# Kernel optimization log

Measured on AMD Instinct MI355X. Metric: run time of the kernel, lower is better.

The kernel has to match this reference:

```python
import jax, jax.numpy as jnp
import numpy as np
import math

_PI = math.pi

@jax.custom_vjp
def atan_spike(h):
    # Heaviside forward, ATan surrogate (alpha=2.0) backward
    return (h >= 0).astype(h.dtype)

def _atan_fwd(h):
    return (h >= 0).astype(h.dtype), h

def _atan_bwd(h, g):
    # d/dh [ (1/pi) atan(pi*h) + 1/2 ] = 1 / (1 + (pi*h)^2)
    return (g / (1.0 + (_PI * h) ** 2),)

atan_spike.defvjp(_atan_fwd, _atan_bwd)

def plif_scan(x, alpha, v_th):
    # x: [T, ...]; PLIF: v += alpha*(x - v); spike; hard reset to 0
    a = alpha.reshape(())
    def step(v, xt):
        v = v + a * (xt - v)
        s = atan_spike(v - v_th)
        v = v * (1.0 - s)
        return v, s
    v0 = jnp.zeros_like(x[0])
    _, spikes = jax.lax.scan(step, v0, x)
    return spikes

def setup_inputs() -> dict:
    key = jax.random.key(0)
    k1, k2, k3 = jax.random.split(key, 3)
    T, B, N, D, H = 4, 8, 1024, 512, 2048
    x = jax.random.normal(k1, (T, B, N, D), dtype=jnp.float32)
    W1 = jax.random.normal(k2, (H, D), dtype=jnp.float32) * (1.0 / math.sqrt(D))
    W2 = jax.random.normal(k3, (D, H), dtype=jnp.float32) * (1.0 / math.sqrt(H))
    alpha1 = jnp.full((1,), 0.5, dtype=jnp.float32)  # 1/tau, tau=2.0
    alpha2 = jnp.full((1,), 0.5, dtype=jnp.float32)
    return {"x": x, "W1": W1, "W2": W2, "alpha1": alpha1, "alpha2": alpha2}

def reference(x, W1, W2, alpha1, alpha2):
    V_TH = 1.0
    h = jnp.einsum('tbnd,hd->tbnh', x, W1)      # fc1 (no bias)
    s1 = plif_scan(h, alpha1, V_TH)             # PLIF neuron 1
    y = jnp.einsum('tbnh,dh->tbnd', s1, W2)     # fc2 (no bias)
    s2 = plif_scan(y, alpha2, V_TH)             # PLIF neuron 2
    return s2
```

## Files before the change

kernel.cpp:

```cpp
#include <hip/hip_runtime.h>

#define T_  4
#define BN_ 8192
#define D_  512
#define H_  2048

typedef float f4 __attribute__((ext_vector_type(4)));
typedef float f32x4 __attribute__((ext_vector_type(4)));
typedef _Float16 f16x8 __attribute__((ext_vector_type(8)));

__device__ __forceinline__ void split8(const f4 u0, const f4 u1, f16x8& hi, f16x8& lo) {
#pragma unroll
    for (int i = 0; i < 4; ++i) {
        _Float16 a = (_Float16)u0[i]; hi[i]     = a; lo[i]     = (_Float16)(u0[i] - (float)a);
        _Float16 b = (_Float16)u1[i]; hi[4 + i] = b; lo[4 + i] = (_Float16)(u1[i] - (float)b);
    }
}

__device__ __forceinline__ void spikes4_to_f16(unsigned b, unsigned& lo, unsigned& hi) {
    const unsigned p0 = (b & 0xFFu) | ((b & 0xFF00u) << 8);
    const unsigned p1 = ((b >> 16) & 0xFFu) | ((b >> 8) & 0xFF0000u);
    lo = p0 * 0x3C00u;
    hi = p1 * 0x3C00u;
}

__device__ __forceinline__ void glds16(const void* g, void* l) {
    __builtin_amdgcn_global_load_lds((const __attribute__((address_space(1))) unsigned int*)g,
                                     (__attribute__((address_space(3))) unsigned int*)l, 16, 0, 0);
}

__global__ __launch_bounds__(256)
void k_split(const float* __restrict__ x, _Float16* __restrict__ xs)
{
    const int b   = blockIdx.x;
    const int t   = b & 3;
    const int k0B = (b >> 2) & 15;
    const int bnB = b >> 6;
    const int kg  = threadIdx.x & 3;
    const int row = threadIdx.x >> 2;

    const float* src = x + ((size_t)t * BN_ + bnB * 64 + row) * D_ + k0B * 32 + kg * 8;
    const f4 u0 = *(const f4*)src;
    const f4 u1 = *(const f4*)(src + 4);
    f16x8 hi, lo;
    split8(u0, u1, hi, lo);

    const size_t base = ((size_t)(bnB * 16 + k0B) * 4 + t) * 4096;
    *(f16x8*)&xs[base +        kg * 512 + row * 8] = hi;
    *(f16x8*)&xs[base + 2048 + kg * 512 + row * 8] = lo;
}

__global__ __launch_bounds__(256)
void k_splitW(const float* __restrict__ W1, _Float16* __restrict__ w1s)
{
    const int gid = blockIdx.x * 256 + threadIdx.x;
    const int col = gid & 127;
    const int kg  = (gid >> 7) & 3;
    const int kb  = (gid >> 9) & 15;
    const int h0b = gid >> 13;

    const float* src = W1 + (size_t)(h0b * 128 + col) * D_ + kb * 32 + kg * 8;
    const f4 u0 = *(const f4*)src;
    const f4 u1 = *(const f4*)(src + 4);
    f16x8 hi, lo;
    split8(u0, u1, hi, lo);

    const size_t base = (size_t)(h0b * 16 + kb) * 8192;
    *(f16x8*)&w1s[base +        kg * 1024 + col * 8] = hi;
    *(f16x8*)&w1s[base + 4096 + kg * 1024 + col * 8] = lo;
}

__global__ __launch_bounds__(256)
void k_splitW2(const float* __restrict__ W2, _Float16* __restrict__ w2s)
{
    const int gid = blockIdx.x * 256 + threadIdx.x;
    const int col = gid & 127;
    const int kg  = (gid >> 7) & 3;
    const int kb  = (gid >> 9) & 63;
    const int d0b = gid >> 15;

    const float* src = W2 + (size_t)(d0b * 128 + col) * H_ + kb * 32 + kg * 8;
    const f4 u0 = *(const f4*)src;
    const f4 u1 = *(const f4*)(src + 4);
    f16x8 hi, lo;
    split8(u0, u1, hi, lo);

    const size_t base = (size_t)(d0b * 64 + kb) * 8192;
    *(f16x8*)&w2s[base +        kg * 1024 + col * 8] = hi;
    *(f16x8*)&w2s[base + 4096 + kg * 1024 + col * 8] = lo;
}

__global__ __launch_bounds__(256, 2)
void k_fc1b(const _Float16* __restrict__ xs, const _Float16* __restrict__ w1s,
            const float* __restrict__ alphap, unsigned char* __restrict__ s1)
{
    __shared__ _Float16 Ab[2][T_][2][4][64][8];

    const int tid  = threadIdx.x;
    const int lane = tid & 63;
    const int w    = tid >> 6;
    const int wr   = (w >> 1) * 32;
    const int wc   = (w & 1) * 64;

    const int gid   = blockIdx.x;
    const int panel = gid >> 8;
    const int h0i   = (gid >> 4) & 15;
    const int bnL   = gid & 15;
    const int bnB   = panel * 16 + bnL;
    const int bn0   = bnB * 64;
    const int h0    = h0i * 128;

    const int l15 = lane & 15;
    const int kgl = lane >> 4;
    const int lq  = kgl * 4;

    const float a1v = alphap[0];

    f32x4 acc[T_][2][4];
#pragma unroll
    for (int t = 0; t < T_; ++t)
#pragma unroll
        for (int m = 0; m < 2; ++m)
#pragma unroll
            for (int n = 0; n < 4; ++n) acc[t][m][n] = (f32x4){0.f, 0.f, 0.f, 0.f};

    const char* xbase = (const char*)xs + (size_t)bnB * 16 * 32768;
    const _Float16* bl = w1s + (size_t)h0i * (16 * 8192)
                             + (size_t)kgl * 1024 + (size_t)(wc + l15) * 8;

#define FC1_GLDS(BUF, KB)                                                        \
    {                                                                            \
        const char* cb_ = xbase + (size_t)(KB) * 32768;                          \
        _Float16* lA_ = &Ab[BUF][0][0][0][0][0];                                 \
        _Pragma("unroll")                                                        \
        for (int i_ = 0; i_ < 8; ++i_) {                                         \
            const int c_ = i_ * 4 + w;                                           \
            glds16(cb_ + c_ * 1024 + lane * 16, lA_ + c_ * 512);                 \
        }                                                                        \
    }

#define FC1_BLOAD(KB, B0, B1)                                                    \
    {                                                                            \
        const _Float16* bp_ = bl + (size_t)(KB) * 8192;                          \
        _Pragma("unroll")                                                        \
        for (int n_ = 0; n_ < 4; ++n_) {                                         \
            B0[n_] = *(const f16x8*)(bp_ + n_ * 128);                            \
            B1[n_] = *(const f16x8*)(bp_ + 4096 + n_ * 128);                     \
        }                                                                        \
    }

#define FC1_COMPUTE(BUF, B0, B1)                                                 \
    _Pragma("unroll")                                                            \
    for (int t_ = 0; t_ < T_; ++t_)                                              \
        _Pragma("unroll")                                                        \
        for (int m_ = 0; m_ < 2; ++m_) {                                         \
            const f16x8 a0_ = *(const f16x8*)&Ab[BUF][t_][0][kgl][wr + m_ * 16 + l15][0]; \
            const f16x8 a1_ = *(const f16x8*)&Ab[BUF][t_][1][kgl][wr + m_ * 16 + l15][0]; \
            _Pragma("unroll")                                                    \
            for (int n_ = 0; n_ < 4; ++n_) {                                     \
                acc[t_][m_][n_] = __builtin_amdgcn_mfma_f32_16x16x32_f16(a0_, B0[n_], acc[t_][m_][n_], 0, 0, 0); \
                acc[t_][m_][n_] = __builtin_amdgcn_mfma_f32_16x16x32_f16(a0_, B1[n_], acc[t_][m_][n_], 0, 0, 0); \
                acc[t_][m_][n_] = __builtin_amdgcn_mfma_f32_16x16x32_f16(a1_, B0[n_], acc[t_][m_][n_], 0, 0, 0); \
            }                                                                    \
        }

    f16x8 bc0[4], bc1[4], bpA0[4], bpA1[4];

    FC1_GLDS(0, 0)
    FC1_BLOAD(0, bc0, bc1)

    int buf = 0;
#pragma unroll 1
    for (int kb = 0; kb < 15; ++kb) {
        __builtin_amdgcn_s_barrier();
        FC1_GLDS(buf ^ 1, kb + 1)
        FC1_BLOAD(kb + 1, bpA0, bpA1)
        asm volatile("s_waitcnt vmcnt(16)" ::: "memory");
        __builtin_amdgcn_sched_barrier(0);
        FC1_COMPUTE(buf, bc0, bc1)
#pragma unroll
        for (int n = 0; n < 4; ++n) { bc0[n] = bpA0[n]; bc1[n] = bpA1[n]; }
        buf ^= 1;
    }
    __builtin_amdgcn_s_barrier();
    asm volatile("s_waitcnt vmcnt(0)" ::: "memory");
    __builtin_amdgcn_sched_barrier(0);
    FC1_COMPUTE(buf, bc0, bc1)

#pragma unroll
    for (int m = 0; m < 2; ++m)
#pragma unroll
        for (int n = 0; n < 4; ++n)
#pragma unroll
            for (int q = 0; q < 4; ++q) {
                float v = 0.f;
#pragma unroll
                for (int t = 0; t < T_; ++t) {
                    v = v + a1v * (acc[t][m][n][q] - v);
                    const bool sp = (v >= 1.0f);
                    s1[((size_t)t * BN_ + bn0 + wr + m * 16 + lq + q) * H_ +
                       (h0 + wc + n * 16 + l15)] = sp ? (unsigned char)1 : (unsigned char)0;
                    if (sp) v = 0.f;
                }
            }
}

__global__ __launch_bounds__(256, 2)
void k_fc1(const _Float16* __restrict__ xs, const float* __restrict__ W1,
           const float* __restrict__ alphap, unsigned char* __restrict__ s1)
{
    __shared__ _Float16 Ab[T_][2][4][64][8];
    __shared__ _Float16 Bb[2][4][128][8];

    const int tid  = threadIdx.x;
    const int lane = tid & 63;
    const int w    = tid >> 6;
    const int wr   = (w >> 1) * 32;
    const int wc   = (w & 1) * 64;
    const int bnB  = blockIdx.x;
    const int bn0  = bnB * 64;
    const int h0   = blockIdx.y * 128;

    const int l15 = lane & 15;
    const int kgl = lane >> 4;
    const int lq  = kgl * 4;

    const int bcol = tid & 127;
    const int bkh  = tid >> 7;

    const float a1v = alphap[0];

    f32x4 acc[T_][2][4];
#pragma unroll
    for (int t = 0; t < T_; ++t)
#pragma unroll
        for (int m = 0; m < 2; ++m)
#pragma unroll
            for (int n = 0; n < 4; ++n) acc[t][m][n] = (f32x4){0.f, 0.f, 0.f, 0.f};

    const char* xbase = (const char*)xs + (size_t)bnB * 16 * 32768;
    const float* wp0  = W1 + (size_t)(h0 + bcol) * D_ + bkh * 16;

    f4 w0 = *(const f4*)wp0,       w1 = *(const f4*)(wp0 + 4);
    f4 w2 = *(const f4*)(wp0 + 8), w3 = *(const f4*)(wp0 + 12);

    for (int kb = 0; kb < 16; ++kb) {
        __syncthreads();
        const char* cb = xbase + (size_t)kb * 32768;
        _Float16* lA = &Ab[0][0][0][0][0];
#pragma unroll
        for (int i = 0; i < 8; ++i) {
            const int c = i * 4 + w;
            glds16(cb + c * 1024 + lane * 16, lA + c * 512);
        }
        {
            f16x8 hA, lA2, hB, lB;
            split8(w0, w1, hA, lA2); split8(w2, w3, hB, lB);
            *(f16x8*)&Bb[0][2 * bkh][bcol][0]     = hA;
            *(f16x8*)&Bb[0][2 * bkh + 1][bcol][0] = hB;
            *(f16x8*)&Bb[1][2 * bkh][bcol][0]     = lA2;
            *(f16x8*)&Bb[1][2 * bkh + 1][bcol][0] = lB;
        }
        if (kb < 15) {
            const float* wp = wp0 + (kb + 1) * 32;
            w0 = *(const f4*)wp;       w1 = *(const f4*)(wp + 4);
            w2 = *(const f4*)(wp + 8); w3 = *(const f4*)(wp + 12);
        }
        __syncthreads();

        f16x8 bf0[4], bf1[4];
#pragma unroll
        for (int n = 0; n < 4; ++n) {
            bf0[n] = *(const f16x8*)&Bb[0][kgl][wc + n * 16 + l15][0];
            bf1[n] = *(const f16x8*)&Bb[1][kgl][wc + n * 16 + l15][0];
        }
#pragma unroll
        for (int t = 0; t < T_; ++t)
#pragma unroll
            for (int m = 0; m < 2; ++m) {
                const f16x8 a0 = *(const f16x8*)&Ab[t][0][kgl][wr + m * 16 + l15][0];
                const f16x8 a1 = *(const f16x8*)&Ab[t][1][kgl][wr + m * 16 + l15][0];
#pragma unroll
                for (int n = 0; n < 4; ++n) {
                    acc[t][m][n] = __builtin_amdgcn_mfma_f32_16x16x32_f16(a0, bf0[n], acc[t][m][n], 0, 0, 0);
                    acc[t][m][n] = __builtin_amdgcn_mfma_f32_16x16x32_f16(a0, bf1[n], acc[t][m][n], 0, 0, 0);
                    acc[t][m][n] = __builtin_amdgcn_mfma_f32_16x16x32_f16(a1, bf0[n], acc[t][m][n], 0, 0, 0);
                }
            }
    }

#pragma unroll
    for (int m = 0; m < 2; ++m)
#pragma unroll
        for (int n = 0; n < 4; ++n)
#pragma unroll
            for (int q = 0; q < 4; ++q) {
                float v = 0.f;
#pragma unroll
                for (int t = 0; t < T_; ++t) {
                    v = v + a1v * (acc[t][m][n][q] - v);
                    const bool sp = (v >= 1.0f);
                    s1[((size_t)t * BN_ + bn0 + wr + m * 16 + lq + q) * H_ +
                       (h0 + wc + n * 16 + l15)] = sp ? (unsigned char)1 : (unsigned char)0;
                    if (sp) v = 0.f;
                }
            }
}

__global__ __launch_bounds__(256, 2)
void k_fc2b(const unsigned char* __restrict__ s1, const _Float16* __restrict__ w2s,
            const float* __restrict__ alphap, float* __restrict__ out)
{
    __shared__ _Float16 A2[2][T_][4][64][8];

    const int tid  = threadIdx.x;
    const int lane = tid & 63;
    const int w    = tid >> 6;
    const int wr   = (w >> 1) * 32;
    const int wc   = (w & 1) * 64;
    const int bn0  = blockIdx.x * 64;
    const int d0i  = blockIdx.y;
    const int d0   = d0i * 128;

    const int l15 = lane & 15;
    const int kgl = lane >> 4;
    const int lq  = kgl * 4;

    const int at   = w;
    const int arow = lane;

    const float a2v = alphap[0];

    f32x4 acc[T_][2][4];
#pragma unroll
    for (int t = 0; t < T_; ++t)
#pragma unroll
        for (int m = 0; m < 2; ++m)
#pragma unroll
            for (int n = 0; n < 4; ++n) acc[t][m][n] = (f32x4){0.f, 0.f, 0.f, 0.f};

    const unsigned char* ap = s1 + ((size_t)at * BN_ + bn0 + arow) * H_;
    const _Float16* bl = w2s + (size_t)d0i * (64 * 8192)
                             + (size_t)kgl * 1024 + (size_t)(wc + l15) * 8;

#define FC2_ACONV_WRITE(BUF, R0, R1)                                             \
    {                                                                            \
        unsigned v_[8];                                                          \
        spikes4_to_f16(R0.x, v_[0], v_[1]); spikes4_to_f16(R0.y, v_[2], v_[3]);  \
        spikes4_to_f16(R0.z, v_[4], v_[5]); spikes4_to_f16(R0.w, v_[6], v_[7]);  \
        *(uint4*)&A2[BUF][at][0][arow][0] = *(const uint4*)&v_[0];               \
        *(uint4*)&A2[BUF][at][1][arow][0] = *(const uint4*)&v_[4];               \
        spikes4_to_f16(R1.x, v_[0], v_[1]); spikes4_to_f16(R1.y, v_[2], v_[3]);  \
        spikes4_to_f16(R1.z, v_[4], v_[5]); spikes4_to_f16(R1.w, v_[6], v_[7]);  \
        *(uint4*)&A2[BUF][at][2][arow][0] = *(const uint4*)&v_[0];               \
        *(uint4*)&A2[BUF][at][3][arow][0] = *(const uint4*)&v_[4];               \
    }

#define FC2_BLOAD(KB, B0, B1)                                                    \
    {                                                                            \
        const _Float16* bp_ = bl + (size_t)(KB) * 8192;                          \
        _Pragma("unroll")                                                        \
        for (int n_ = 0; n_ < 4; ++n_) {                                         \
            B0[n_] = *(const f16x8*)(bp_ + n_ * 128);                            \
            B1[n_] = *(const f16x8*)(bp_ + 4096 + n_ * 128);                     \
        }                                                                        \
    }

    f16x8 bc0[4], bc1[4], bpA0[4], bpA1[4];

    {
        const uint4 r0 = *(const uint4*)(ap);
        const uint4 r1 = *(const uint4*)(ap + 16);
        FC2_ACONV_WRITE(0, r0, r1)
        FC2_BLOAD(0, bc0, bc1)
    }
    __syncthreads();

    int cur = 0;
    for (int kb = 0; kb < 64; ++kb) {
        uint4 r0, r1;
        if (kb < 63) {
            r0 = *(const uint4*)(ap + (kb + 1) * 32);
            r1 = *(const uint4*)(ap + (kb + 1) * 32 + 16);
            FC2_BLOAD(kb + 1, bpA0, bpA1)
        }

#pragma unroll
        for (int t = 0; t < T_; ++t)
#pragma unroll
            for (int m = 0; m < 2; ++m) {
                const f16x8 af = *(const f16x8*)&A2[cur][t][kgl][wr + m * 16 + l15][0];
#pragma unroll
                for (int n = 0; n < 4; ++n) {
                    acc[t][m][n] = __builtin_amdgcn_mfma_f32_16x16x32_f16(af, bc0[n], acc[t][m][n], 0, 0, 0);
                    acc[t][m][n] = __builtin_amdgcn_mfma_f32_16x16x32_f16(af, bc1[n], acc[t][m][n], 0, 0, 0);
                }
            }

        if (kb < 63) {
            FC2_ACONV_WRITE(cur ^ 1, r0, r1)
        }
        __syncthreads();
        if (kb < 63) {
#pragma unroll
            for (int n = 0; n < 4; ++n) { bc0[n] = bpA0[n]; bc1[n] = bpA1[n]; }
        }
        cur ^= 1;
    }

#pragma unroll
    for (int m = 0; m < 2; ++m)
#pragma unroll
        for (int n = 0; n < 4; ++n)
#pragma unroll
            for (int q = 0; q < 4; ++q) {
                float v = 0.f;
#pragma unroll
                for (int t = 0; t < T_; ++t) {
                    v = v + a2v * (acc[t][m][n][q] - v);
                    const bool sp = (v >= 1.0f);
                    out[((size_t)t * BN_ + bn0 + wr + m * 16 + lq + q) * D_ +
                        (d0 + wc + n * 16 + l15)] = sp ? 1.0f : 0.0f;
                    if (sp) v = 0.f;
                }
            }
}

__global__ __launch_bounds__(256, 2)
void k_fc2(const unsigned char* __restrict__ s1, const float* __restrict__ W2,
           const float* __restrict__ alphap, float* __restrict__ out)
{
    __shared__ _Float16 A2[2][4][4][64][8];
    __shared__ _Float16 B2[2][2][4][128][8];

    const int tid  = threadIdx.x;
    const int lane = tid & 63;
    const int w    = tid >> 6;
    const int wr   = (w >> 1) * 32;
    const int wc   = (w & 1) * 64;
    const int bn0  = blockIdx.x * 64;
    const int d0   = blockIdx.y * 128;

    const int l15 = lane & 15;
    const int kgl = lane >> 4;
    const int lq  = kgl * 4;

    const int bcol = tid & 127;
    const int bkh  = tid >> 7;
    const int at   = tid >> 6;
    const int arow = lane;

    const float a2v = alphap[0];

    f32x4 acc[T_][2][4];
#pragma unroll
    for (int t = 0; t < T_; ++t)
#pragma unroll
        for (int m = 0; m < 2; ++m)
#pragma unroll
            for (int n = 0; n < 4; ++n) acc[t][m][n] = (f32x4){0.f, 0.f, 0.f, 0.f};

    const unsigned char* ap = s1 + ((size_t)at * BN_ + bn0 + arow) * H_;
    const float*         wp0 = W2 + (size_t)(d0 + bcol) * H_ + bkh * 16;

    {
        const uint4 r0 = *(const uint4*)(ap);
        const uint4 r1 = *(const uint4*)(ap + 16);
        unsigned v[8];
        spikes4_to_f16(r0.x, v[0], v[1]); spikes4_to_f16(r0.y, v[2], v[3]);
        spikes4_to_f16(r0.z, v[4], v[5]); spikes4_to_f16(r0.w, v[6], v[7]);
        *(uint4*)&A2[0][at][0][arow][0] = *(const uint4*)&v[0];
        *(uint4*)&A2[0][at][1][arow][0] = *(const uint4*)&v[4];
        spikes4_to_f16(r1.x, v[0], v[1]); spikes4_to_f16(r1.y, v[2], v[3]);
        spikes4_to_f16(r1.z, v[4], v[5]); spikes4_to_f16(r1.w, v[6], v[7]);
        *(uint4*)&A2[0][at][2][arow][0] = *(const uint4*)&v[0];
        *(uint4*)&A2[0][at][3][arow][0] = *(const uint4*)&v[4];

        const f4 w0 = *(const f4*)wp0, w1 = *(const f4*)(wp0 + 4);
        const f4 w2 = *(const f4*)(wp0 + 8), w3 = *(const f4*)(wp0 + 12);
        f16x8 hA, lA, hB, lB;
        split8(w0, w1, hA, lA); split8(w2, w3, hB, lB);
        *(f16x8*)&B2[0][0][2 * bkh][bcol][0]     = hA;
        *(f16x8*)&B2[0][0][2 * bkh + 1][bcol][0] = hB;
        *(f16x8*)&B2[0][1][2 * bkh][bcol][0]     = lA;
        *(f16x8*)&B2[0][1][2 * bkh + 1][bcol][0] = lB;
    }
    __syncthreads();

    int cur = 0;
    for (int kb = 0; kb < 64; ++kb) {
        uint4 r0, r1; f4 w0, w1, w2, w3;
        if (kb < 63) {
            r0 = *(const uint4*)(ap + (kb + 1) * 32);
            r1 = *(const uint4*)(ap + (kb + 1) * 32 + 16);
            const float* wp = wp0 + (kb + 1) * 32;
            w0 = *(const f4*)wp;       w1 = *(const f4*)(wp + 4);
            w2 = *(const f4*)(wp + 8); w3 = *(const f4*)(wp + 12);
        }

        f16x8 bf0[4], bf1[4];
#pragma unroll
        for (int n = 0; n < 4; ++n) {
            bf0[n] = *(const f16x8*)&B2[cur][0][kgl][wc + n * 16 + l15][0];
            bf1[n] = *(const f16x8*)&B2[cur][1][kgl][wc + n * 16 + l15][0];
        }
#pragma unroll
        for (int t = 0; t < T_; ++t)
#pragma unroll
            for (int m = 0; m < 2; ++m) {
                const f16x8 af = *(const f16x8*)&A2[cur][t][kgl][wr + m * 16 + l15][0];
#pragma unroll
                for (int n = 0; n < 4; ++n) {
                    acc[t][m][n] = __builtin_amdgcn_mfma_f32_16x16x32_f16(af, bf0[n], acc[t][m][n], 0, 0, 0);
                    acc[t][m][n] = __builtin_amdgcn_mfma_f32_16x16x32_f16(af, bf1[n], acc[t][m][n], 0, 0, 0);
                }
            }

        if (kb < 63) {
            unsigned v[8];
            spikes4_to_f16(r0.x, v[0], v[1]); spikes4_to_f16(r0.y, v[2], v[3]);
            spikes4_to_f16(r0.z, v[4], v[5]); spikes4_to_f16(r0.w, v[6], v[7]);
            *(uint4*)&A2[cur ^ 1][at][0][arow][0] = *(const uint4*)&v[0];
            *(uint4*)&A2[cur ^ 1][at][1][arow][0] = *(const uint4*)&v[4];
            spikes4_to_f16(r1.x, v[0], v[1]); spikes4_to_f16(r1.y, v[2], v[3]);
            spikes4_to_f16(r1.z, v[4], v[5]); spikes4_to_f16(r1.w, v[6], v[7]);
            *(uint4*)&A2[cur ^ 1][at][2][arow][0] = *(const uint4*)&v[0];
            *(uint4*)&A2[cur ^ 1][at][3][arow][0] = *(const uint4*)&v[4];

            f16x8 hA, lA, hB, lB;
            split8(w0, w1, hA, lA); split8(w2, w3, hB, lB);
            *(f16x8*)&B2[cur ^ 1][0][2 * bkh][bcol][0]     = hA;
            *(f16x8*)&B2[cur ^ 1][0][2 * bkh + 1][bcol][0] = hB;
            *(f16x8*)&B2[cur ^ 1][1][2 * bkh][bcol][0]     = lA;
            *(f16x8*)&B2[cur ^ 1][1][2 * bkh + 1][bcol][0] = lB;
        }
        __syncthreads();
        cur ^= 1;
    }

#pragma unroll
    for (int m = 0; m < 2; ++m)
#pragma unroll
        for (int n = 0; n < 4; ++n)
#pragma unroll
            for (int q = 0; q < 4; ++q) {
                float v = 0.f;
#pragma unroll
                for (int t = 0; t < T_; ++t) {
                    v = v + a2v * (acc[t][m][n][q] - v);
                    const bool sp = (v >= 1.0f);
                    out[((size_t)t * BN_ + bn0 + wr + m * 16 + lq + q) * D_ +
                        (d0 + wc + n * 16 + l15)] = sp ? 1.0f : 0.0f;
                    if (sp) v = 0.f;
                }
            }
}

extern "C" void kernel_launch(void* const* d_in, const int* in_sizes, int n_in,
                              void* d_out, int out_size, void* d_ws, size_t ws_size,
                              hipStream_t stream) {
    const float* x      = (const float*)d_in[0];
    const float* W1     = (const float*)d_in[1];
    const float* W2     = (const float*)d_in[2];
    const float* alpha1 = (const float*)d_in[3];
    const float* alpha2 = (const float*)d_in[4];
    float* out = (float*)d_out;

    unsigned char* s1 = (unsigned char*)d_ws;
    _Float16* xs = (_Float16*)d_out;
    const size_t S1_BYTES  = (size_t)T_ * BN_ * H_;
    const size_t W1S_BYTES = (size_t)H_ * D_ * 2 * sizeof(_Float16);
    const size_t W2S_BYTES = (size_t)D_ * H_ * 2 * sizeof(_Float16);

    k_split<<<dim3(8192), dim3(256), 0, stream>>>(x, xs);

    const bool haveW1 = ws_size >= S1_BYTES + W1S_BYTES;
    const bool haveW2 = ws_size >= S1_BYTES + W1S_BYTES + W2S_BYTES;

    if (haveW1) {
        _Float16* w1s = (_Float16*)((char*)d_ws + S1_BYTES);
        k_splitW<<<dim3(512), dim3(256), 0, stream>>>(W1, w1s);
        k_fc1b<<<dim3(2048), dim3(256), 0, stream>>>(xs, w1s, alpha1, s1);
    } else {
        k_fc1<<<dim3(128, 16), dim3(256), 0, stream>>>(xs, W1, alpha1, s1);
    }

    if (haveW2) {
        _Float16* w2s = (_Float16*)((char*)d_ws + S1_BYTES + W1S_BYTES);
        k_splitW2<<<dim3(512), dim3(256), 0, stream>>>(W2, w2s);
        k_fc2b<<<dim3(128, 4), dim3(256), 0, stream>>>(s1, w2s, alpha2, out);
    } else {
        k_fc2<<<dim3(128, 4), dim3(256), 0, stream>>>(s1, W2, alpha2, out);
    }
}
```

Before: 293.7 us.

## Shrink fc1 tile to 32 rows, raise occupancy, unroll double-buffer ping-pong

The fc1 kernel now computes a 32x128 output tile per block with each wave covering 32 columns, in place of 64x128. That halves accumulator registers and LDS, so launch bounds can request 4 blocks per CU and the grid doubles to 4096 blocks. The x split layout is changed to 32-row panels to match. The K loop is unrolled by two with fixed ping-pong LDS buffers and tighter vmcnt waits. The fallback k_fc1 path and the W1 workspace check are removed, which assumes the workspace is always large enough. Smaller tiles also lower data reuse per block.

After: 300.8 us. 2.4% more time.

```diff
diff --git a/kernel.cpp b/kernel.cpp
--- a/kernel.cpp
+++ b/kernel.cpp
@@ -32,22 +32,24 @@
 __global__ __launch_bounds__(256)
 void k_split(const float* __restrict__ x, _Float16* __restrict__ xs)
 {
-    const int b   = blockIdx.x;
-    const int t   = b & 3;
-    const int k0B = (b >> 2) & 15;
-    const int bnB = b >> 6;
-    const int kg  = threadIdx.x & 3;
-    const int row = threadIdx.x >> 2;
-
-    const float* src = x + ((size_t)t * BN_ + bnB * 64 + row) * D_ + k0B * 32 + kg * 8;
+    const int b     = blockIdx.x;
+    const int t     = b & 3;
+    const int k0B   = (b >> 2) & 15;
+    const int bnB64 = b >> 6;
+    const int kg    = threadIdx.x & 3;
+    const int row64 = threadIdx.x >> 2;
+
+    const float* src = x + ((size_t)t * BN_ + bnB64 * 64 + row64) * D_ + k0B * 32 + kg * 8;
     const f4 u0 = *(const f4*)src;
     const f4 u1 = *(const f4*)(src + 4);
     f16x8 hi, lo;
     split8(u0, u1, hi, lo);
 
-    const size_t base = ((size_t)(bnB * 16 + k0B) * 4 + t) * 4096;
-    *(f16x8*)&xs[base +        kg * 512 + row * 8] = hi;
-    *(f16x8*)&xs[base + 2048 + kg * 512 + row * 8] = lo;
+    const int bnB32 = bnB64 * 2 + (row64 >> 5);
+    const int r     = row64 & 31;
+    const size_t base = (size_t)(bnB32 * 16 + k0B) * 8192 + t * 2048;
+    *(f16x8*)&xs[base +        kg * 256 + r * 8] = hi;
+    *(f16x8*)&xs[base + 1024 + kg * 256 + r * 8] = lo;
 }
 
 __global__ __launch_bounds__(256)
@@ -90,24 +92,23 @@
     *(f16x8*)&w2s[base + 4096 + kg * 1024 + col * 8] = lo;
 }
 
-__global__ __launch_bounds__(256, 2)
+__global__ __launch_bounds__(256, 4)
 void k_fc1b(const _Float16* __restrict__ xs, const _Float16* __restrict__ w1s,
             const float* __restrict__ alphap, unsigned char* __restrict__ s1)
 {
-    __shared__ _Float16 Ab[2][T_][2][4][64][8];
+    __shared__ _Float16 Ab[2][T_][2][4][32][8];
 
     const int tid  = threadIdx.x;
     const int lane = tid & 63;
     const int w    = tid >> 6;
-    const int wr   = (w >> 1) * 32;
-    const int wc   = (w & 1) * 64;
+    const int wc   = w * 32;
 
     const int gid   = blockIdx.x;
     const int panel = gid >> 8;
     const int h0i   = (gid >> 4) & 15;
     const int bnL   = gid & 15;
     const int bnB   = panel * 16 + bnL;
-    const int bn0   = bnB * 64;
+    const int bn0   = bnB * 32;
     const int h0    = h0i * 128;
 
     const int l15 = lane & 15;
@@ -116,37 +117,36 @@
 
     const float a1v = alphap[0];
 
-    f32x4 acc[T_][2][4];
+    f32x4 acc[T_][2][2];
 #pragma unroll
     for (int t = 0; t < T_; ++t)
 #pragma unroll
         for (int m = 0; m < 2; ++m)
 #pragma unroll
-            for (int n = 0; n < 4; ++n) acc[t][m][n] = (f32x4){0.f, 0.f, 0.f, 0.f};
-
-    const char* xbase = (const char*)xs + (size_t)bnB * 16 * 32768;
+            for (int n = 0; n < 2; ++n) acc[t][m][n] = (f32x4){0.f, 0.f, 0.f, 0.f};
+
+    const char* xbase = (const char*)xs + (size_t)bnB * 16 * 16384;
     const _Float16* bl = w1s + (size_t)h0i * (16 * 8192)
                              + (size_t)kgl * 1024 + (size_t)(wc + l15) * 8;
 
 #define FC1_GLDS(BUF, KB)                                                        \
     {                                                                            \
-        const char* cb_ = xbase + (size_t)(KB) * 32768;                          \
+        const char* cb_ = xbase + (size_t)(KB) * 16384;                          \
         _Float16* lA_ = &Ab[BUF][0][0][0][0][0];                                 \
         _Pragma("unroll")                                                        \
-        for (int i_ = 0; i_ < 8; ++i_) {                                         \
-            const int c_ = i_ * 4 + w;                                           \
-            glds16(cb_ + c_ * 1024 + lane * 16, lA_ + c_ * 512);                 \
+        for (int i_ = 0; i_ < 4; ++i_) {                                         \
+            const int s_ = i_ * 4 + w;                                           \
+            glds16(cb_ + s_ * 1024 + lane * 16, lA_ + s_ * 512);                 \
         }                                                                        \
     }
 
 #define FC1_BLOAD(KB, B0, B1)                                                    \
     {                                                                            \
         const _Float16* bp_ = bl + (size_t)(KB) * 8192;                          \
-        _Pragma("unroll")                                                        \
-        for (int n_ = 0; n_ < 4; ++n_) {                                         \
-            B0[n_] = *(const f16x8*)(bp_ + n_ * 128);                            \
-            B1[n_] = *(const f16x8*)(bp_ + 4096 + n_ * 128);                     \
-        }                                                                        \
+        B0[0] = *(const f16x8*)(bp_);                                            \
+        B0[1] = *(const f16x8*)(bp_ + 128);                                      \
+        B1[0] = *(const f16x8*)(bp_ + 4096);                                     \
+        B1[1] = *(const f16x8*)(bp_ + 4096 + 128);                               \
     }
 
 #define FC1_COMPUTE(BUF, B0, B1)                                                 \
@@ -154,43 +154,49 @@
     for (int t_ = 0; t_ < T_; ++t_)                                              \
         _Pragma("unroll")                                                        \
         for (int m_ = 0; m_ < 2; ++m_) {                                         \
-            const f16x8 a0_ = *(const f16x8*)&Ab[BUF][t_][0][kgl][wr + m_ * 16 + l15][0]; \
-            const f16x8 a1_ = *(const f16x8*)&Ab[BUF][t_][1][kgl][wr + m_ * 16 + l15][0]; \
+            const f16x8 a0_ = *(const f16x8*)&Ab[BUF][t_][0][kgl][m_ * 16 + l15][0]; \
+            const f16x8 a1_ = *(const f16x8*)&Ab[BUF][t_][1][kgl][m_ * 16 + l15][0]; \
             _Pragma("unroll")                                                    \
-            for (int n_ = 0; n_ < 4; ++n_) {                                     \
+            for (int n_ = 0; n_ < 2; ++n_) {                                     \
                 acc[t_][m_][n_] = __builtin_amdgcn_mfma_f32_16x16x32_f16(a0_, B0[n_], acc[t_][m_][n_], 0, 0, 0); \
                 acc[t_][m_][n_] = __builtin_amdgcn_mfma_f32_16x16x32_f16(a0_, B1[n_], acc[t_][m_][n_], 0, 0, 0); \
                 acc[t_][m_][n_] = __builtin_amdgcn_mfma_f32_16x16x32_f16(a1_, B0[n_], acc[t_][m_][n_], 0, 0, 0); \
             }                                                                    \
         }
 
-    f16x8 bc0[4], bc1[4], bpA0[4], bpA1[4];
-
+    f16x8 bA0[2], bA1[2], bB0[2], bB1[2];
+
+    FC1_BLOAD(0, bA0, bA1)
+    __builtin_amdgcn_sched_barrier(0);
     FC1_GLDS(0, 0)
-    FC1_BLOAD(0, bc0, bc1)
-
-    int buf = 0;
+
 #pragma unroll 1
-    for (int kb = 0; kb < 15; ++kb) {
+    for (int it = 0; it < 8; ++it) {
+        const int kb = 2 * it;
         __builtin_amdgcn_s_barrier();
-        FC1_GLDS(buf ^ 1, kb + 1)
-        FC1_BLOAD(kb + 1, bpA0, bpA1)
-        asm volatile("s_waitcnt vmcnt(16)" ::: "memory");
+        FC1_BLOAD(kb + 1, bB0, bB1)
         __builtin_amdgcn_sched_barrier(0);
-        FC1_COMPUTE(buf, bc0, bc1)
-#pragma unroll
-        for (int n = 0; n < 4; ++n) { bc0[n] = bpA0[n]; bc1[n] = bpA1[n]; }
-        buf ^= 1;
-    }
-    __builtin_amdgcn_s_barrier();
-    asm volatile("s_waitcnt vmcnt(0)" ::: "memory");
-    __builtin_amdgcn_sched_barrier(0);
-    FC1_COMPUTE(buf, bc0, bc1)
+        FC1_GLDS(1, kb + 1)
+        asm volatile("s_waitcnt vmcnt(8)" ::: "memory");
+        __builtin_amdgcn_sched_barrier(0);
+        FC1_COMPUTE(0, bA0, bA1)
+        __builtin_amdgcn_s_barrier();
+        if (it < 7) {
+            FC1_BLOAD(kb + 2, bA0, bA1)
+            __builtin_amdgcn_sched_barrier(0);
+            FC1_GLDS(0, kb + 2)
+            asm volatile("s_waitcnt vmcnt(8)" ::: "memory");
+        } else {
+            asm volatile("s_waitcnt vmcnt(0)" ::: "memory");
+        }
+        __builtin_amdgcn_sched_barrier(0);
+        FC1_COMPUTE(1, bB0, bB1)
+    }
 
 #pragma unroll
     for (int m = 0; m < 2; ++m)
 #pragma unroll
-        for (int n = 0; n < 4; ++n)
+        for (int n = 0; n < 2; ++n)
 #pragma unroll
             for (int q = 0; q < 4; ++q) {
                 float v = 0.f;
@@ -198,109 +204,7 @@
                 for (int t = 0; t < T_; ++t) {
                     v = v + a1v * (acc[t][m][n][q] - v);
                     const bool sp = (v >= 1.0f);
-                    s1[((size_t)t * BN_ + bn0 + wr + m * 16 + lq + q) * H_ +
-                       (h0 + wc + n * 16 + l15)] = sp ? (unsigned char)1 : (unsigned char)0;
-                    if (sp) v = 0.f;
-                }
-            }
-}
-
-__global__ __launch_bounds__(256, 2)
-void k_fc1(const _Float16* __restrict__ xs, const float* __restrict__ W1,
-           const float* __restrict__ alphap, unsigned char* __restrict__ s1)
-{
-    __shared__ _Float16 Ab[T_][2][4][64][8];
-    __shared__ _Float16 Bb[2][4][128][8];
-
-    const int tid  = threadIdx.x;
-    const int lane = tid & 63;
-    const int w    = tid >> 6;
-    const int wr   = (w >> 1) * 32;
-    const int wc   = (w & 1) * 64;
-    const int bnB  = blockIdx.x;
-    const int bn0  = bnB * 64;
-    const int h0   = blockIdx.y * 128;
-
-    const int l15 = lane & 15;
-    const int kgl = lane >> 4;
-    const int lq  = kgl * 4;
-
-    const int bcol = tid & 127;
-    const int bkh  = tid >> 7;
-
-    const float a1v = alphap[0];
-
-    f32x4 acc[T_][2][4];
-#pragma unroll
-    for (int t = 0; t < T_; ++t)
-#pragma unroll
-        for (int m = 0; m < 2; ++m)
-#pragma unroll
-            for (int n = 0; n < 4; ++n) acc[t][m][n] = (f32x4){0.f, 0.f, 0.f, 0.f};
-
-    const char* xbase = (const char*)xs + (size_t)bnB * 16 * 32768;
-    const float* wp0  = W1 + (size_t)(h0 + bcol) * D_ + bkh * 16;
-
-    f4 w0 = *(const f4*)wp0,       w1 = *(const f4*)(wp0 + 4);
-    f4 w2 = *(const f4*)(wp0 + 8), w3 = *(const f4*)(wp0 + 12);
-
-    for (int kb = 0; kb < 16; ++kb) {
-        __syncthreads();
-        const char* cb = xbase + (size_t)kb * 32768;
-        _Float16* lA = &Ab[0][0][0][0][0];
-#pragma unroll
-        for (int i = 0; i < 8; ++i) {
-            const int c = i * 4 + w;
-            glds16(cb + c * 1024 + lane * 16, lA + c * 512);
-        }
-        {
-            f16x8 hA, lA2, hB, lB;
-            split8(w0, w1, hA, lA2); split8(w2, w3, hB, lB);
-            *(f16x8*)&Bb[0][2 * bkh][bcol][0]     = hA;
-            *(f16x8*)&Bb[0][2 * bkh + 1][bcol][0] = hB;
-            *(f16x8*)&Bb[1][2 * bkh][bcol][0]     = lA2;
-            *(f16x8*)&Bb[1][2 * bkh + 1][bcol][0] = lB;
-        }
-        if (kb < 15) {
-            const float* wp = wp0 + (kb + 1) * 32;
-            w0 = *(const f4*)wp;       w1 = *(const f4*)(wp + 4);
-            w2 = *(const f4*)(wp + 8); w3 = *(const f4*)(wp + 12);
-        }
-        __syncthreads();
-
-        f16x8 bf0[4], bf1[4];
-#pragma unroll
-        for (int n = 0; n < 4; ++n) {
-            bf0[n] = *(const f16x8*)&Bb[0][kgl][wc + n * 16 + l15][0];
-            bf1[n] = *(const f16x8*)&Bb[1][kgl][wc + n * 16 + l15][0];
-        }
-#pragma unroll
-        for (int t = 0; t < T_; ++t)
-#pragma unroll
-            for (int m = 0; m < 2; ++m) {
-                const f16x8 a0 = *(const f16x8*)&Ab[t][0][kgl][wr + m * 16 + l15][0];
-                const f16x8 a1 = *(const f16x8*)&Ab[t][1][kgl][wr + m * 16 + l15][0];
-#pragma unroll
-                for (int n = 0; n < 4; ++n) {
-                    acc[t][m][n] = __builtin_amdgcn_mfma_f32_16x16x32_f16(a0, bf0[n], acc[t][m][n], 0, 0, 0);
-                    acc[t][m][n] = __builtin_amdgcn_mfma_f32_16x16x32_f16(a0, bf1[n], acc[t][m][n], 0, 0, 0);
-                    acc[t][m][n] = __builtin_amdgcn_mfma_f32_16x16x32_f16(a1, bf0[n], acc[t][m][n], 0, 0, 0);
-                }
-            }
-    }
-
-#pragma unroll
-    for (int m = 0; m < 2; ++m)
-#pragma unroll
-        for (int n = 0; n < 4; ++n)
-#pragma unroll
-            for (int q = 0; q < 4; ++q) {
-                float v = 0.f;
-#pragma unroll
-                for (int t = 0; t < T_; ++t) {
-                    v = v + a1v * (acc[t][m][n][q] - v);
-                    const bool sp = (v >= 1.0f);
-                    s1[((size_t)t * BN_ + bn0 + wr + m * 16 + lq + q) * H_ +
+                    s1[((size_t)t * BN_ + bn0 + m * 16 + lq + q) * H_ +
                        (h0 + wc + n * 16 + l15)] = sp ? (unsigned char)1 : (unsigned char)0;
                     if (sp) v = 0.f;
                 }
@@ -574,18 +478,11 @@
 
     k_split<<<dim3(8192), dim3(256), 0, stream>>>(x, xs);
 
-    const bool haveW1 = ws_size >= S1_BYTES + W1S_BYTES;
-    const bool haveW2 = ws_size >= S1_BYTES + W1S_BYTES + W2S_BYTES;
-
-    if (haveW1) {
-        _Float16* w1s = (_Float16*)((char*)d_ws + S1_BYTES);
-        k_splitW<<<dim3(512), dim3(256), 0, stream>>>(W1, w1s);
-        k_fc1b<<<dim3(2048), dim3(256), 0, stream>>>(xs, w1s, alpha1, s1);
-    } else {
-        k_fc1<<<dim3(128, 16), dim3(256), 0, stream>>>(xs, W1, alpha1, s1);
-    }
-
-    if (haveW2) {
+    _Float16* w1s = (_Float16*)((char*)d_ws + S1_BYTES);
+    k_splitW<<<dim3(512), dim3(256), 0, stream>>>(W1, w1s);
+    k_fc1b<<<dim3(4096), dim3(256), 0, stream>>>(xs, w1s, alpha1, s1);
+
+    if (ws_size >= S1_BYTES + W1S_BYTES + W2S_BYTES) {
         _Float16* w2s = (_Float16*)((char*)d_ws + S1_BYTES + W1S_BYTES);
         k_splitW2<<<dim3(512), dim3(256), 0, stream>>>(W2, w2s);
         k_fc2b<<<dim3(128, 4), dim3(256), 0, stream>>>(s1, w2s, alpha2, out);
```
